# Kernel tuning notes

Measured on AMD Instinct MI355X. Metric: run time of the kernel, lower is better.

## Reference

```python
import jax, jax.numpy as jnp
import numpy as np

EMBED_DIM = 1024
NUM_HEADS = 16
DEPTH = EMBED_DIM // NUM_HEADS  # 64
B, S = 4, 2048


def setup_inputs() -> dict:
    key = jax.random.key(0)
    ks = jax.random.split(key, 12)
    sc = 0.02
    return {
        "q": jax.random.normal(ks[0], (B, S, EMBED_DIM), jnp.float32),
        "k": jax.random.normal(ks[1], (B, S, EMBED_DIM), jnp.float32),
        "v": jax.random.normal(ks[2], (B, S, EMBED_DIM), jnp.float32),
        # per-head Dense(depth) weights stacked over heads: [H, D, depth]
        "wq": jax.random.normal(ks[3], (NUM_HEADS, EMBED_DIM, DEPTH), jnp.float32) * sc,
        "bq": jnp.zeros((NUM_HEADS, DEPTH), jnp.float32),
        "wk": jax.random.normal(ks[4], (NUM_HEADS, EMBED_DIM, DEPTH), jnp.float32) * sc,
        "bk": jnp.zeros((NUM_HEADS, DEPTH), jnp.float32),
        "wv": jax.random.normal(ks[5], (NUM_HEADS, EMBED_DIM, DEPTH), jnp.float32) * sc,
        "bv": jnp.zeros((NUM_HEADS, DEPTH), jnp.float32),
        # final Dense(embedding_dim): [D, D]
        "wo": jax.random.normal(ks[6], (EMBED_DIM, EMBED_DIM), jnp.float32) * sc,
        "bo": jnp.zeros((EMBED_DIM,), jnp.float32),
        "use_mask": 1,
    }


def reference(q, k, v, wq, bq, wk, bk, wv, bv, wo, bo, use_mask):
    # Batched per-head projections (equivalent to H separate Dense layers).
    qh = jnp.einsum('bsd,hde->bhse', q, wq) + bq[None, :, None, :]
    kh = jnp.einsum('bsd,hde->bhse', k, wk) + bk[None, :, None, :]
    vh = jnp.einsum('bsd,hde->bhse', v, wv) + bv[None, :, None, :]

    scale = 1.0 / jnp.sqrt(jnp.asarray(DEPTH, jnp.float32))
    logits = jnp.einsum('bhqe,bhke->bhqk', qh, kh) * scale  # [B,H,Sq,Sk]
    if use_mask:
        Sq, Sk = qh.shape[2], kh.shape[2]
        causal = jnp.triu(jnp.ones((Sq, Sk), jnp.float32), k=1)
        logits = logits + causal[None, None, :, :] * (-1e9)
    attn = jax.nn.softmax(logits, axis=-1)
    out_h = jnp.einsum('bhqk,bhke->bhqe', attn, vh)  # [B,H,Sq,depth]
    # concat heads along last dim -> [B,Sq,H*depth]
    bsz, H, Sq, dep = out_h.shape
    concat = out_h.transpose(0, 2, 1, 3).reshape(bsz, Sq, H * dep)
    return concat @ wo + bo
```

## Files before the change

### kernel.cpp

```cpp
#include <hip/hip_runtime.h>

#define B_ 4
#define S_ 2048
#define H_ 16
#define D_ 64
#define E_ 1024
#define M_ 8192

typedef __attribute__((ext_vector_type(8))) __bf16 bf16x8;
typedef __attribute__((ext_vector_type(4))) __bf16 bf16x4;
typedef __attribute__((ext_vector_type(4))) float f32x4;
typedef __attribute__((ext_vector_type(16))) float f32x16;

__device__ __forceinline__ void gload_lds16(const void* g, void* l) {
  __builtin_amdgcn_global_load_lds(
      (const __attribute__((address_space(1))) unsigned int*)g,
      (__attribute__((address_space(3))) unsigned int*)l, 16, 0, 0);
}

__device__ __forceinline__ unsigned pk2(float a, float b) {
  union { __bf16 h; unsigned short u; } ua, ub;
  ua.h = (__bf16)a; ub.h = (__bf16)b;
  return ((unsigned)ub.u << 16) | (unsigned)ua.u;
}

__global__ void cvt_all(const float* __restrict__ q, const float* __restrict__ k,
                        const float* __restrict__ v, __bf16* __restrict__ Aq,
                        __bf16* __restrict__ Ak, __bf16* __restrict__ Av) {
  const int y = blockIdx.y;
  const float* src = (y == 0) ? q : (y == 1) ? k : v;
  __bf16* dst = (y == 0) ? Aq : (y == 1) ? Ak : Av;
  const int i = blockIdx.x * blockDim.x + threadIdx.x;
  const float4 vv = ((const float4*)src)[i];
  bf16x4 o;
  o.x = (__bf16)vv.x; o.y = (__bf16)vv.y; o.z = (__bf16)vv.z; o.w = (__bf16)vv.w;
  ((bf16x4*)dst)[i] = o;
}

__global__ void pack_all(const float* __restrict__ wq, const float* __restrict__ wk,
                         const float* __restrict__ wv, const float* __restrict__ wo,
                         __bf16* __restrict__ Bq, __bf16* __restrict__ Bk,
                         __bf16* __restrict__ Bv, __bf16* __restrict__ Bo) {
  const int y = blockIdx.y;
  const int idx = blockIdx.x * 256 + threadIdx.x;
  const int n = idx >> 10, kk = idx & 1023;
  if (y < 3) {
    const float* w = (y == 0) ? wq : (y == 1) ? wk : wv;
    __bf16* out = (y == 0) ? Bq : (y == 1) ? Bk : Bv;
    out[idx] = (__bf16)w[((size_t)(n >> 6) << 16) + (kk << 6) + (n & 63)];
  } else {
    Bo[idx] = (__bf16)wo[((size_t)kk << 10) + n];
  }
}

__global__ __launch_bounds__(256) void gemm_qk(
    const __bf16* __restrict__ Aq, const __bf16* __restrict__ Ak,
    const __bf16* __restrict__ Bq, const __bf16* __restrict__ Bk,
    const float* __restrict__ bq, const float* __restrict__ bk,
    __bf16* __restrict__ qhb, __bf16* __restrict__ khb) {
  constexpr int K = 1024;
  __shared__ __bf16 As[128 * 64];
  __shared__ __bf16 Bs[128 * 64];
  const int t = threadIdx.x;
  const int w = t >> 6, l = t & 63;
  const int isK = blockIdx.y >> 3;
  const __bf16* A = isK ? Ak : Aq;
  const __bf16* Bt = isK ? Bk : Bq;
  const float* bias = isK ? bk : bq;
  __bf16* C = isK ? khb : qhb;
  const int m0 = blockIdx.x * 128, n0 = (blockIdx.y & 7) * 128;
  f32x4 acc[4][4] = {};

  for (int kt = 0; kt < K / 64; ++kt) {
    const int kb = kt * 64;
#pragma unroll
    for (int j = 0; j < 4; ++j) {
      const int ci = (j * 4 + w) * 64 + l;
      const int row = ci >> 3;
      const int c = (ci & 7) ^ (row & 7);
      gload_lds16(A + (size_t)(m0 + row) * K + kb + c * 8, As + (j * 4 + w) * 512);
      gload_lds16(Bt + (size_t)(n0 + row) * K + kb + c * 8, Bs + (j * 4 + w) * 512);
    }
    __syncthreads();
#pragma unroll
    for (int kk = 0; kk < 64; kk += 32) {
      bf16x8 af[4], bfr[4];
#pragma unroll
      for (int f = 0; f < 4; ++f) {
        const int ra = (w >> 1) * 64 + f * 16 + (l & 15);
        const int ca = ((kk >> 3) + (l >> 4)) ^ (ra & 7);
        af[f] = *(const bf16x8*)(As + ra * 64 + ca * 8);
        const int rb = (w & 1) * 64 + f * 16 + (l & 15);
        const int cb = ((kk >> 3) + (l >> 4)) ^ (rb & 7);
        bfr[f] = *(const bf16x8*)(Bs + rb * 64 + cb * 8);
      }
#pragma unroll
      for (int mf = 0; mf < 4; ++mf)
#pragma unroll
        for (int nf = 0; nf < 4; ++nf)
          acc[mf][nf] = __builtin_amdgcn_mfma_f32_16x16x32_bf16(af[mf], bfr[nf],
                                                                acc[mf][nf], 0, 0, 0);
    }
    __syncthreads();
  }

#pragma unroll
  for (int mf = 0; mf < 4; ++mf)
#pragma unroll
    for (int nf = 0; nf < 4; ++nf)
#pragma unroll
      for (int r = 0; r < 4; ++r) {
        const int gm = m0 + (w >> 1) * 64 + mf * 16 + (l >> 4) * 4 + r;
        const int gn = n0 + (w & 1) * 64 + nf * 16 + (l & 15);
        const float val = acc[mf][nf][r] + bias[gn];
        C[(((size_t)(gm >> 11) * H_ + (gn >> 6)) * S_ + (gm & 2047)) * D_ + (gn & 63)] =
            (__bf16)val;
      }
}

template <int MODE>
__global__ __launch_bounds__(256) void gemm_bt(const __bf16* __restrict__ A,
                                               const __bf16* __restrict__ Bt,
                                               const float* __restrict__ bias,
                                               void* __restrict__ Cout) {
  constexpr int K = 1024;
  __shared__ __bf16 As[128 * 64];
  __shared__ __bf16 Bs[128 * 64];
  const int t = threadIdx.x;
  const int w = t >> 6, l = t & 63;
  const int m0 = blockIdx.x * 128, n0 = blockIdx.y * 128;
  f32x4 acc[4][4] = {};

  for (int kt = 0; kt < K / 64; ++kt) {
    const int kb = kt * 64;
#pragma unroll
    for (int j = 0; j < 4; ++j) {
      const int ci = (j * 4 + w) * 64 + l;
      const int row = ci >> 3;
      const int c = (ci & 7) ^ (row & 7);
      gload_lds16(A + (size_t)(m0 + row) * K + kb + c * 8, As + (j * 4 + w) * 512);
      gload_lds16(Bt + (size_t)(n0 + row) * K + kb + c * 8, Bs + (j * 4 + w) * 512);
    }
    __syncthreads();
#pragma unroll
    for (int kk = 0; kk < 64; kk += 32) {
      bf16x8 af[4], bfr[4];
#pragma unroll
      for (int f = 0; f < 4; ++f) {
        const int ra = (w >> 1) * 64 + f * 16 + (l & 15);
        const int ca = ((kk >> 3) + (l >> 4)) ^ (ra & 7);
        af[f] = *(const bf16x8*)(As + ra * 64 + ca * 8);
        const int rb = (w & 1) * 64 + f * 16 + (l & 15);
        const int cb = ((kk >> 3) + (l >> 4)) ^ (rb & 7);
        bfr[f] = *(const bf16x8*)(Bs + rb * 64 + cb * 8);
      }
#pragma unroll
      for (int mf = 0; mf < 4; ++mf)
#pragma unroll
        for (int nf = 0; nf < 4; ++nf)
          acc[mf][nf] = __builtin_amdgcn_mfma_f32_16x16x32_bf16(af[mf], bfr[nf],
                                                                acc[mf][nf], 0, 0, 0);
    }
    __syncthreads();
  }

#pragma unroll
  for (int mf = 0; mf < 4; ++mf) {
#pragma unroll
    for (int nf = 0; nf < 4; ++nf) {
#pragma unroll
      for (int r = 0; r < 4; ++r) {
        const int gm = m0 + (w >> 1) * 64 + mf * 16 + (l >> 4) * 4 + r;
        const int gn = n0 + (w & 1) * 64 + nf * 16 + (l & 15);
        const float val = acc[mf][nf][r] + ((MODE == 1) ? bias[gm] : bias[gn]);
        if constexpr (MODE == 1) {
          ((__bf16*)Cout)[(((size_t)(gn >> 11) * H_ + (gm >> 6)) * D_ + (gm & 63)) * S_ + (gn & 2047)] =
              (__bf16)val;
        } else {
          ((float*)Cout)[(size_t)gm * 1024 + gn] = val;
        }
      }
    }
  }
}

__global__ __launch_bounds__(256, 2) void attn_fused(const __bf16* __restrict__ qh,
                                                     const __bf16* __restrict__ kh,
                                                     const __bf16* __restrict__ vT,
                                                     __bf16* __restrict__ concat,
                                                     const int* __restrict__ use_mask_p) {
  __shared__ __bf16 Ks[2][64 * 64];
  __shared__ __bf16 Vs[2][64 * 64];
  const int t = threadIdx.x, w = t >> 6, l = t & 63;
  const int lo = l & 31, hi = l >> 5;
  const int bh = blockIdx.x, pr = blockIdx.y;
  const int usemask = *use_mask_p;
  const __bf16* Qb = qh + (size_t)bh * S_ * D_;
  const __bf16* Kb = kh + (size_t)bh * S_ * D_;
  const __bf16* Vb = vT + (size_t)bh * D_ * S_;
  const int b = bh >> 4, hh = bh & 15;
  constexpr float CEXP = 0.125f * 1.4426950408889634f;

  int cur = 0;
  for (int half = 0; half < 2; ++half) {
    const int qt = half ? (15 - pr) : pr;
    const int qrow0 = qt * 128 + w * 32;
    const int nkt = usemask ? (2 * qt + 2) : (S_ / 64);
    const int ktw = usemask ? (2 * qt + (w >> 1)) : 100000;
    const int ktdiag = usemask ? (2 * qt + (w >> 1)) : -1;

    bf16x8 qf[4];
#pragma unroll
    for (int ks = 0; ks < 4; ++ks)
      qf[ks] = *(const bf16x8*)(Qb + (size_t)(qrow0 + lo) * D_ + ks * 16 + hi * 8);

    float m = -3e38f, ls = 0.f;
    f32x16 o0 = {}, o1 = {};

#pragma unroll
    for (int j = 0; j < 2; ++j) {
      const int ci = j * 256 + t;
      const int row = ci >> 3;
      const int sc = (ci & 7) ^ (row & 7);
      gload_lds16(Kb + (size_t)row * D_ + sc * 8, &Ks[cur][j * 2048 + w * 512]);
      gload_lds16(Vb + (size_t)row * S_ + sc * 8, &Vs[cur][j * 2048 + w * 512]);
    }

    for (int kt = 0; kt < nkt; ++kt) {
      __builtin_amdgcn_sched_barrier(0);
      asm volatile("s_waitcnt vmcnt(0)" ::: "memory");
      __builtin_amdgcn_s_barrier();
      __builtin_amdgcn_sched_barrier(0);

      if (kt + 1 < nkt) {
        const int nxt = cur ^ 1;
#pragma unroll
        for (int j = 0; j < 2; ++j) {
          const int ci = j * 256 + t;
          const int row = ci >> 3;
          const int sc = (ci & 7) ^ (row & 7);
          gload_lds16(Kb + (size_t)((kt + 1) * 64 + row) * D_ + sc * 8,
                      &Ks[nxt][j * 2048 + w * 512]);
          gload_lds16(Vb + (size_t)row * S_ + (kt + 1) * 64 + sc * 8,
                      &Vs[nxt][j * 2048 + w * 512]);
        }
      }

      if (kt <= ktw) {
        f32x16 s0 = {}, s1 = {};
        __builtin_amdgcn_s_setprio(1);
#pragma unroll
        for (int ks = 0; ks < 4; ++ks) {
          const int ch = ((ks << 1) | hi) ^ (lo & 7);
          const bf16x8 k0 = *(const bf16x8*)(&Ks[cur][lo * 64 + ch * 8]);
          const bf16x8 k1 = *(const bf16x8*)(&Ks[cur][(32 + lo) * 64 + ch * 8]);
          s0 = __builtin_amdgcn_mfma_f32_32x32x16_bf16(k0, qf[ks], s0, 0, 0, 0);
          s1 = __builtin_amdgcn_mfma_f32_32x32x16_bf16(k1, qf[ks], s1, 0, 0, 0);
        }
        __builtin_amdgcn_s_setprio(0);

        if (kt == ktdiag) {
          const int qloc = ((w & 1) << 5) + lo;
#pragma unroll
          for (int r = 0; r < 16; ++r) {
            const int kv0 = (r & 3) + 8 * (r >> 2) + 4 * hi;
            if (kv0 > qloc) s0[r] = -1e30f;
            if (kv0 + 32 > qloc) s1[r] = -1e30f;
          }
        }

        float pm = s0[0];
#pragma unroll
        for (int r = 1; r < 16; ++r) pm = fmaxf(pm, s0[r]);
#pragma unroll
        for (int r = 0; r < 16; ++r) pm = fmaxf(pm, s1[r]);
        pm = fmaxf(pm, __shfl_xor(pm, 32));

        if (!__all(pm - m <= 64.0f)) {
          const float mn = fmaxf(m, pm);
          const float al = __builtin_amdgcn_exp2f((m - mn) * CEXP);
          m = mn;
          ls *= al;
          o0 *= al;
          o1 *= al;
        }
        const float mneg = -m * CEXP;

        unsigned W0[4][2], W1[4][2];
        float rs0 = 0.f, rs1 = 0.f;
#pragma unroll
        for (int j = 0; j < 4; ++j) {
          float p0 = __builtin_amdgcn_exp2f(__builtin_fmaf(s0[4 * j + 0], CEXP, mneg));
          float p1 = __builtin_amdgcn_exp2f(__builtin_fmaf(s0[4 * j + 1], CEXP, mneg));
          float p2 = __builtin_amdgcn_exp2f(__builtin_fmaf(s0[4 * j + 2], CEXP, mneg));
          float p3 = __builtin_amdgcn_exp2f(__builtin_fmaf(s0[4 * j + 3], CEXP, mneg));
          rs0 += (p0 + p1) + (p2 + p3);
          W0[j][0] = pk2(p0, p1);
          W0[j][1] = pk2(p2, p3);
          float q0 = __builtin_amdgcn_exp2f(__builtin_fmaf(s1[4 * j + 0], CEXP, mneg));
          float q1 = __builtin_amdgcn_exp2f(__builtin_fmaf(s1[4 * j + 1], CEXP, mneg));
          float q2 = __builtin_amdgcn_exp2f(__builtin_fmaf(s1[4 * j + 2], CEXP, mneg));
          float q3 = __builtin_amdgcn_exp2f(__builtin_fmaf(s1[4 * j + 3], CEXP, mneg));
          rs1 += (q0 + q1) + (q2 + q3);
          W1[j][0] = pk2(q0, q1);
          W1[j][1] = pk2(q2, q3);
        }
        float rs = rs0 + rs1;
        rs += __shfl_xor(rs, 32);
        ls += rs;

        bf16x8 pa[4];
#pragma unroll
        for (int ks = 0; ks < 4; ++ks) {
          const int c = ks & 1;
          unsigned x0, x1, y0, y1;
          if ((ks >> 1) == 0) {
            x0 = W0[2 * c][0]; x1 = W0[2 * c][1];
            y0 = W0[2 * c + 1][0]; y1 = W0[2 * c + 1][1];
          } else {
            x0 = W1[2 * c][0]; x1 = W1[2 * c][1];
            y0 = W1[2 * c + 1][0]; y1 = W1[2 * c + 1][1];
          }
          asm volatile("v_permlane32_swap_b32 %0, %1" : "+v"(x0), "+v"(y0));
          asm volatile("v_permlane32_swap_b32 %0, %1" : "+v"(x1), "+v"(y1));
          union { unsigned u[4]; bf16x8 v; } uu;
          uu.u[0] = x0; uu.u[1] = x1; uu.u[2] = y0; uu.u[3] = y1;
          pa[ks] = uu.v;
        }

        __builtin_amdgcn_s_setprio(1);
#pragma unroll
        for (int ks = 0; ks < 4; ++ks) {
          const int ch = ((ks << 1) | hi) ^ (lo & 7);
          const bf16x8 v0 = *(const bf16x8*)(&Vs[cur][lo * 64 + ch * 8]);
          const bf16x8 v1 = *(const bf16x8*)(&Vs[cur][(32 + lo) * 64 + ch * 8]);
          o0 = __builtin_amdgcn_mfma_f32_32x32x16_bf16(v0, pa[ks], o0, 0, 0, 0);
          o1 = __builtin_amdgcn_mfma_f32_32x32x16_bf16(v1, pa[ks], o1, 0, 0, 0);
        }
        __builtin_amdgcn_s_setprio(0);
      }
      cur ^= 1;
    }

    const float inv = 1.0f / ls;
    const size_t rowbase = ((size_t)(b * S_ + qrow0 + lo)) * E_ + hh * 64;
#pragma unroll
    for (int rr = 0; rr < 4; ++rr) {
      bf16x4 v0, v1;
#pragma unroll
      for (int bb = 0; bb < 4; ++bb) {
        v0[bb] = (__bf16)(o0[4 * rr + bb] * inv);
        v1[bb] = (__bf16)(o1[4 * rr + bb] * inv);
      }
      *(bf16x4*)(concat + rowbase + 8 * rr + 4 * hi) = v0;
      *(bf16x4*)(concat + rowbase + 32 + 8 * rr + 4 * hi) = v1;
    }
  }
}

extern "C" void kernel_launch(void* const* d_in, const int* in_sizes, int n_in,
                              void* d_out, int out_size, void* d_ws, size_t ws_size,
                              hipStream_t stream) {
  const float* q = (const float*)d_in[0];
  const float* k = (const float*)d_in[1];
  const float* v = (const float*)d_in[2];
  const float* wq = (const float*)d_in[3];
  const float* bq = (const float*)d_in[4];
  const float* wk = (const float*)d_in[5];
  const float* bk = (const float*)d_in[6];
  const float* wv = (const float*)d_in[7];
  const float* bv = (const float*)d_in[8];
  const float* wo = (const float*)d_in[9];
  const float* bo = (const float*)d_in[10];
  const int* use_mask = (const int*)d_in[11];
  (void)in_sizes; (void)n_in; (void)out_size; (void)ws_size;

  char* ws = (char*)d_ws;
  __bf16* Aq = (__bf16*)ws;
  __bf16* Ak = Aq + (size_t)M_ * E_;
  __bf16* Av = Ak + (size_t)M_ * E_;
  __bf16* Bq = Av + (size_t)M_ * E_;
  __bf16* Bk = Bq + (size_t)E_ * E_;
  __bf16* Bv = Bk + (size_t)E_ * E_;
  __bf16* Bo = Bv + (size_t)E_ * E_;
  __bf16* qhb = Bo + (size_t)E_ * E_;
  __bf16* khb = qhb + (size_t)8388608;
  __bf16* vTb = khb + (size_t)8388608;
  __bf16* concat = Aq;

  cvt_all<<<dim3(8192, 3), 256, 0, stream>>>(q, k, v, Aq, Ak, Av);
  pack_all<<<dim3(4096, 4), 256, 0, stream>>>(wq, wk, wv, wo, Bq, Bk, Bv, Bo);
  gemm_qk<<<dim3(64, 16), 256, 0, stream>>>(Aq, Ak, Bq, Bk, bq, bk, qhb, khb);
  gemm_bt<1><<<dim3(8, 64), 256, 0, stream>>>(Bv, Av, bv, vTb);
  attn_fused<<<dim3(64, 8), 256, 0, stream>>>(qhb, khb, vTb, concat, use_mask);
  gemm_bt<2><<<dim3(64, 8), 256, 0, stream>>>(concat, Bo, bo, d_out);
}
```

Before: 197.9 us.

## Merge Q/K/V projection GEMMs into one launch and split attention into one q-tile per block

The V-projection GEMM is folded into the Q/K projection kernel as a third grid segment, so the three projections run in one 1536-block launch instead of two. The attention kernel no longer pairs a light and a heavy causal q-tile inside each block. It launches one block per q-tile (1024 blocks), with heavy tiles scheduled first by reversing blockIdx.y. This aims to cut launch overhead and improve load balance and occupancy, but gives up the explicit pairing that kept per-block causal work even.

Result: slower. 208.6 us (+5.4%).

```diff
diff --git a/kernel.cpp b/kernel.cpp
--- a/kernel.cpp
+++ b/kernel.cpp
@@ -53,24 +53,29 @@
   }
 }
 
-__global__ __launch_bounds__(256) void gemm_qk(
+__global__ __launch_bounds__(256) void gemm_qkv(
     const __bf16* __restrict__ Aq, const __bf16* __restrict__ Ak,
-    const __bf16* __restrict__ Bq, const __bf16* __restrict__ Bk,
+    const __bf16* __restrict__ Av, const __bf16* __restrict__ Bq,
+    const __bf16* __restrict__ Bk, const __bf16* __restrict__ Bv,
     const float* __restrict__ bq, const float* __restrict__ bk,
-    __bf16* __restrict__ qhb, __bf16* __restrict__ khb) {
+    const float* __restrict__ bv, __bf16* __restrict__ qhb,
+    __bf16* __restrict__ khb, __bf16* __restrict__ vTb) {
   constexpr int K = 1024;
   __shared__ __bf16 As[128 * 64];
   __shared__ __bf16 Bs[128 * 64];
   const int t = threadIdx.x;
   const int w = t >> 6, l = t & 63;
-  const int isK = blockIdx.y >> 3;
-  const __bf16* A = isK ? Ak : Aq;
-  const __bf16* Bt = isK ? Bk : Bq;
-  const float* bias = isK ? bk : bq;
-  __bf16* C = isK ? khb : qhb;
-  const int m0 = blockIdx.x * 128, n0 = (blockIdx.y & 7) * 128;
+  const int seg = blockIdx.y >> 3;
+  const int yy = blockIdx.y & 7;
+  const __bf16 *A, *Bt;
+  const float* bias;
+  __bf16* C;
+  int m0, n0;
+  if (seg == 0) { A = Aq; Bt = Bq; bias = bq; C = qhb; m0 = blockIdx.x * 128; n0 = yy * 128; }
+  else if (seg == 1) { A = Ak; Bt = Bk; bias = bk; C = khb; m0 = blockIdx.x * 128; n0 = yy * 128; }
+  else { A = Bv; Bt = Av; bias = bv; C = vTb; m0 = yy * 128; n0 = blockIdx.x * 128; }
+
   f32x4 acc[4][4] = {};
-
   for (int kt = 0; kt < K / 64; ++kt) {
     const int kb = kt * 64;
 #pragma unroll
@@ -105,24 +110,31 @@
   }
 
 #pragma unroll
-  for (int mf = 0; mf < 4; ++mf)
-#pragma unroll
-    for (int nf = 0; nf < 4; ++nf)
+  for (int mf = 0; mf < 4; ++mf) {
+#pragma unroll
+    for (int nf = 0; nf < 4; ++nf) {
 #pragma unroll
       for (int r = 0; r < 4; ++r) {
         const int gm = m0 + (w >> 1) * 64 + mf * 16 + (l >> 4) * 4 + r;
         const int gn = n0 + (w & 1) * 64 + nf * 16 + (l & 15);
-        const float val = acc[mf][nf][r] + bias[gn];
-        C[(((size_t)(gm >> 11) * H_ + (gn >> 6)) * S_ + (gm & 2047)) * D_ + (gn & 63)] =
-            (__bf16)val;
-      }
-}
-
-template <int MODE>
-__global__ __launch_bounds__(256) void gemm_bt(const __bf16* __restrict__ A,
-                                               const __bf16* __restrict__ Bt,
-                                               const float* __restrict__ bias,
-                                               void* __restrict__ Cout) {
+        if (seg < 2) {
+          const float val = acc[mf][nf][r] + bias[gn];
+          C[(((size_t)(gm >> 11) * H_ + (gn >> 6)) * S_ + (gm & 2047)) * D_ + (gn & 63)] =
+              (__bf16)val;
+        } else {
+          const float val = acc[mf][nf][r] + bias[gm];
+          C[(((size_t)(gn >> 11) * H_ + (gm >> 6)) * D_ + (gm & 63)) * S_ + (gn & 2047)] =
+              (__bf16)val;
+        }
+      }
+    }
+  }
+}
+
+__global__ __launch_bounds__(256) void out_gemm(const __bf16* __restrict__ A,
+                                                const __bf16* __restrict__ Bt,
+                                                const float* __restrict__ bias,
+                                                float* __restrict__ Cout) {
   constexpr int K = 1024;
   __shared__ __bf16 As[128 * 64];
   __shared__ __bf16 Bs[128 * 64];
@@ -165,23 +177,15 @@
   }
 
 #pragma unroll
-  for (int mf = 0; mf < 4; ++mf) {
-#pragma unroll
-    for (int nf = 0; nf < 4; ++nf) {
+  for (int mf = 0; mf < 4; ++mf)
+#pragma unroll
+    for (int nf = 0; nf < 4; ++nf)
 #pragma unroll
       for (int r = 0; r < 4; ++r) {
         const int gm = m0 + (w >> 1) * 64 + mf * 16 + (l >> 4) * 4 + r;
         const int gn = n0 + (w & 1) * 64 + nf * 16 + (l & 15);
-        const float val = acc[mf][nf][r] + ((MODE == 1) ? bias[gm] : bias[gn]);
-        if constexpr (MODE == 1) {
-          ((__bf16*)Cout)[(((size_t)(gn >> 11) * H_ + (gm >> 6)) * D_ + (gm & 63)) * S_ + (gn & 2047)] =
-              (__bf16)val;
-        } else {
-          ((float*)Cout)[(size_t)gm * 1024 + gn] = val;
-        }
-      }
-    }
-  }
+        Cout[(size_t)gm * 1024 + gn] = acc[mf][nf][r] + bias[gn];
+      }
 }
 
 __global__ __launch_bounds__(256, 2) void attn_fused(const __bf16* __restrict__ qh,
@@ -193,7 +197,8 @@
   __shared__ __bf16 Vs[2][64 * 64];
   const int t = threadIdx.x, w = t >> 6, l = t & 63;
   const int lo = l & 31, hi = l >> 5;
-  const int bh = blockIdx.x, pr = blockIdx.y;
+  const int bh = blockIdx.x;
+  const int qt = 15 - blockIdx.y;
   const int usemask = *use_mask_p;
   const __bf16* Qb = qh + (size_t)bh * S_ * D_;
   const __bf16* Kb = kh + (size_t)bh * S_ * D_;
@@ -201,160 +206,157 @@
   const int b = bh >> 4, hh = bh & 15;
   constexpr float CEXP = 0.125f * 1.4426950408889634f;
 
+  const int qrow0 = qt * 128 + w * 32;
+  const int nkt = usemask ? (2 * qt + 2) : (S_ / 64);
+  const int ktw = usemask ? (2 * qt + (w >> 1)) : 100000;
+  const int ktdiag = usemask ? (2 * qt + (w >> 1)) : -1;
+
+  bf16x8 qf[4];
+#pragma unroll
+  for (int ks = 0; ks < 4; ++ks)
+    qf[ks] = *(const bf16x8*)(Qb + (size_t)(qrow0 + lo) * D_ + ks * 16 + hi * 8);
+
+  float m = -3e38f, ls = 0.f;
+  f32x16 o0 = {}, o1 = {};
   int cur = 0;
-  for (int half = 0; half < 2; ++half) {
-    const int qt = half ? (15 - pr) : pr;
-    const int qrow0 = qt * 128 + w * 32;
-    const int nkt = usemask ? (2 * qt + 2) : (S_ / 64);
-    const int ktw = usemask ? (2 * qt + (w >> 1)) : 100000;
-    const int ktdiag = usemask ? (2 * qt + (w >> 1)) : -1;
-
-    bf16x8 qf[4];
-#pragma unroll
-    for (int ks = 0; ks < 4; ++ks)
-      qf[ks] = *(const bf16x8*)(Qb + (size_t)(qrow0 + lo) * D_ + ks * 16 + hi * 8);
-
-    float m = -3e38f, ls = 0.f;
-    f32x16 o0 = {}, o1 = {};
-
-#pragma unroll
-    for (int j = 0; j < 2; ++j) {
-      const int ci = j * 256 + t;
-      const int row = ci >> 3;
-      const int sc = (ci & 7) ^ (row & 7);
-      gload_lds16(Kb + (size_t)row * D_ + sc * 8, &Ks[cur][j * 2048 + w * 512]);
-      gload_lds16(Vb + (size_t)row * S_ + sc * 8, &Vs[cur][j * 2048 + w * 512]);
-    }
-
-    for (int kt = 0; kt < nkt; ++kt) {
-      __builtin_amdgcn_sched_barrier(0);
-      asm volatile("s_waitcnt vmcnt(0)" ::: "memory");
-      __builtin_amdgcn_s_barrier();
-      __builtin_amdgcn_sched_barrier(0);
-
-      if (kt + 1 < nkt) {
-        const int nxt = cur ^ 1;
-#pragma unroll
-        for (int j = 0; j < 2; ++j) {
-          const int ci = j * 256 + t;
-          const int row = ci >> 3;
-          const int sc = (ci & 7) ^ (row & 7);
-          gload_lds16(Kb + (size_t)((kt + 1) * 64 + row) * D_ + sc * 8,
-                      &Ks[nxt][j * 2048 + w * 512]);
-          gload_lds16(Vb + (size_t)row * S_ + (kt + 1) * 64 + sc * 8,
-                      &Vs[nxt][j * 2048 + w * 512]);
+
+#pragma unroll
+  for (int j = 0; j < 2; ++j) {
+    const int ci = j * 256 + t;
+    const int row = ci >> 3;
+    const int sc = (ci & 7) ^ (row & 7);
+    gload_lds16(Kb + (size_t)row * D_ + sc * 8, &Ks[cur][j * 2048 + w * 512]);
+    gload_lds16(Vb + (size_t)row * S_ + sc * 8, &Vs[cur][j * 2048 + w * 512]);
+  }
+
+  for (int kt = 0; kt < nkt; ++kt) {
+    __builtin_amdgcn_sched_barrier(0);
+    asm volatile("s_waitcnt vmcnt(0)" ::: "memory");
+    __builtin_amdgcn_s_barrier();
+    __builtin_amdgcn_sched_barrier(0);
+
+    if (kt + 1 < nkt) {
+      const int nxt = cur ^ 1;
+#pragma unroll
+      for (int j = 0; j < 2; ++j) {
+        const int ci = j * 256 + t;
+        const int row = ci >> 3;
+        const int sc = (ci & 7) ^ (row & 7);
+        gload_lds16(Kb + (size_t)((kt + 1) * 64 + row) * D_ + sc * 8,
+                    &Ks[nxt][j * 2048 + w * 512]);
+        gload_lds16(Vb + (size_t)row * S_ + (kt + 1) * 64 + sc * 8,
+                    &Vs[nxt][j * 2048 + w * 512]);
+      }
+    }
+
+    if (kt <= ktw) {
+      f32x16 s0 = {}, s1 = {};
+      __builtin_amdgcn_s_setprio(1);
+#pragma unroll
+      for (int ks = 0; ks < 4; ++ks) {
+        const int ch = ((ks << 1) | hi) ^ (lo & 7);
+        const bf16x8 k0 = *(const bf16x8*)(&Ks[cur][lo * 64 + ch * 8]);
+        const bf16x8 k1 = *(const bf16x8*)(&Ks[cur][(32 + lo) * 64 + ch * 8]);
+        s0 = __builtin_amdgcn_mfma_f32_32x32x16_bf16(k0, qf[ks], s0, 0, 0, 0);
+        s1 = __builtin_amdgcn_mfma_f32_32x32x16_bf16(k1, qf[ks], s1, 0, 0, 0);
+      }
+      __builtin_amdgcn_s_setprio(0);
+
+      if (kt == ktdiag) {
+        const int qloc = ((w & 1) << 5) + lo;
+#pragma unroll
+        for (int r = 0; r < 16; ++r) {
+          const int kv0 = (r & 3) + 8 * (r >> 2) + 4 * hi;
+          if (kv0 > qloc) s0[r] = -1e30f;
+          if (kv0 + 32 > qloc) s1[r] = -1e30f;
         }
       }
 
-      if (kt <= ktw) {
-        f32x16 s0 = {}, s1 = {};
-        __builtin_amdgcn_s_setprio(1);
-#pragma unroll
-        for (int ks = 0; ks < 4; ++ks) {
-          const int ch = ((ks << 1) | hi) ^ (lo & 7);
-          const bf16x8 k0 = *(const bf16x8*)(&Ks[cur][lo * 64 + ch * 8]);
-          const bf16x8 k1 = *(const bf16x8*)(&Ks[cur][(32 + lo) * 64 + ch * 8]);
-          s0 = __builtin_amdgcn_mfma_f32_32x32x16_bf16(k0, qf[ks], s0, 0, 0, 0);
-          s1 = __builtin_amdgcn_mfma_f32_32x32x16_bf16(k1, qf[ks], s1, 0, 0, 0);
+      float pm = s0[0];
+#pragma unroll
+      for (int r = 1; r < 16; ++r) pm = fmaxf(pm, s0[r]);
+#pragma unroll
+      for (int r = 0; r < 16; ++r) pm = fmaxf(pm, s1[r]);
+      pm = fmaxf(pm, __shfl_xor(pm, 32));
+
+      if (!__all(pm - m <= 64.0f)) {
+        const float mn = fmaxf(m, pm);
+        const float al = __builtin_amdgcn_exp2f((m - mn) * CEXP);
+        m = mn;
+        ls *= al;
+        o0 *= al;
+        o1 *= al;
+      }
+      const float mneg = -m * CEXP;
+
+      unsigned W0[4][2], W1[4][2];
+      float rs0 = 0.f, rs1 = 0.f;
+#pragma unroll
+      for (int j = 0; j < 4; ++j) {
+        float p0 = __builtin_amdgcn_exp2f(__builtin_fmaf(s0[4 * j + 0], CEXP, mneg));
+        float p1 = __builtin_amdgcn_exp2f(__builtin_fmaf(s0[4 * j + 1], CEXP, mneg));
+        float p2 = __builtin_amdgcn_exp2f(__builtin_fmaf(s0[4 * j + 2], CEXP, mneg));
+        float p3 = __builtin_amdgcn_exp2f(__builtin_fmaf(s0[4 * j + 3], CEXP, mneg));
+        rs0 += (p0 + p1) + (p2 + p3);
+        W0[j][0] = pk2(p0, p1);
+        W0[j][1] = pk2(p2, p3);
+        float q0 = __builtin_amdgcn_exp2f(__builtin_fmaf(s1[4 * j + 0], CEXP, mneg));
+        float q1 = __builtin_amdgcn_exp2f(__builtin_fmaf(s1[4 * j + 1], CEXP, mneg));
+        float q2 = __builtin_amdgcn_exp2f(__builtin_fmaf(s1[4 * j + 2], CEXP, mneg));
+        float q3 = __builtin_amdgcn_exp2f(__builtin_fmaf(s1[4 * j + 3], CEXP, mneg));
+        rs1 += (q0 + q1) + (q2 + q3);
+        W1[j][0] = pk2(q0, q1);
+        W1[j][1] = pk2(q2, q3);
+      }
+      float rs = rs0 + rs1;
+      rs += __shfl_xor(rs, 32);
+      ls += rs;
+
+      bf16x8 pa[4];
+#pragma unroll
+      for (int ks = 0; ks < 4; ++ks) {
+        const int c = ks & 1;
+        unsigned x0, x1, y0, y1;
+        if ((ks >> 1) == 0) {
+          x0 = W0[2 * c][0]; x1 = W0[2 * c][1];
+          y0 = W0[2 * c + 1][0]; y1 = W0[2 * c + 1][1];
+        } else {
+          x0 = W1[2 * c][0]; x1 = W1[2 * c][1];
+          y0 = W1[2 * c + 1][0]; y1 = W1[2 * c + 1][1];
         }
-        __builtin_amdgcn_s_setprio(0);
-
-        if (kt == ktdiag) {
-          const int qloc = ((w & 1) << 5) + lo;
-#pragma unroll
-          for (int r = 0; r < 16; ++r) {
-            const int kv0 = (r & 3) + 8 * (r >> 2) + 4 * hi;
-            if (kv0 > qloc) s0[r] = -1e30f;
-            if (kv0 + 32 > qloc) s1[r] = -1e30f;
-          }
-        }
-
-        float pm = s0[0];
-#pragma unroll
-        for (int r = 1; r < 16; ++r) pm = fmaxf(pm, s0[r]);
-#pragma unroll
-        for (int r = 0; r < 16; ++r) pm = fmaxf(pm, s1[r]);
-        pm = fmaxf(pm, __shfl_xor(pm, 32));
-
-        if (!__all(pm - m <= 64.0f)) {
-          const float mn = fmaxf(m, pm);
-          const float al = __builtin_amdgcn_exp2f((m - mn) * CEXP);
-          m = mn;
-          ls *= al;
-          o0 *= al;
-          o1 *= al;
-        }
-        const float mneg = -m * CEXP;
-
-        unsigned W0[4][2], W1[4][2];
-        float rs0 = 0.f, rs1 = 0.f;
-#pragma unroll
-        for (int j = 0; j < 4; ++j) {
-          float p0 = __builtin_amdgcn_exp2f(__builtin_fmaf(s0[4 * j + 0], CEXP, mneg));
-          float p1 = __builtin_amdgcn_exp2f(__builtin_fmaf(s0[4 * j + 1], CEXP, mneg));
-          float p2 = __builtin_amdgcn_exp2f(__builtin_fmaf(s0[4 * j + 2], CEXP, mneg));
-          float p3 = __builtin_amdgcn_exp2f(__builtin_fmaf(s0[4 * j + 3], CEXP, mneg));
-          rs0 += (p0 + p1) + (p2 + p3);
-          W0[j][0] = pk2(p0, p1);
-          W0[j][1] = pk2(p2, p3);
-          float q0 = __builtin_amdgcn_exp2f(__builtin_fmaf(s1[4 * j + 0], CEXP, mneg));
-          float q1 = __builtin_amdgcn_exp2f(__builtin_fmaf(s1[4 * j + 1], CEXP, mneg));
-          float q2 = __builtin_amdgcn_exp2f(__builtin_fmaf(s1[4 * j + 2], CEXP, mneg));
-          float q3 = __builtin_amdgcn_exp2f(__builtin_fmaf(s1[4 * j + 3], CEXP, mneg));
-          rs1 += (q0 + q1) + (q2 + q3);
-          W1[j][0] = pk2(q0, q1);
-          W1[j][1] = pk2(q2, q3);
-        }
-        float rs = rs0 + rs1;
-        rs += __shfl_xor(rs, 32);
-        ls += rs;
-
-        bf16x8 pa[4];
-#pragma unroll
-        for (int ks = 0; ks < 4; ++ks) {
-          const int c = ks & 1;
-          unsigned x0, x1, y0, y1;
-          if ((ks >> 1) == 0) {
-            x0 = W0[2 * c][0]; x1 = W0[2 * c][1];
-            y0 = W0[2 * c + 1][0]; y1 = W0[2 * c + 1][1];
-          } else {
-            x0 = W1[2 * c][0]; x1 = W1[2 * c][1];
-            y0 = W1[2 * c + 1][0]; y1 = W1[2 * c + 1][1];
-          }
-          asm volatile("v_permlane32_swap_b32 %0, %1" : "+v"(x0), "+v"(y0));
-          asm volatile("v_permlane32_swap_b32 %0, %1" : "+v"(x1), "+v"(y1));
-          union { unsigned u[4]; bf16x8 v; } uu;
-          uu.u[0] = x0; uu.u[1] = x1; uu.u[2] = y0; uu.u[3] = y1;
-          pa[ks] = uu.v;
-        }
-
-        __builtin_amdgcn_s_setprio(1);
-#pragma unroll
-        for (int ks = 0; ks < 4; ++ks) {
-          const int ch = ((ks << 1) | hi) ^ (lo & 7);
-          const bf16x8 v0 = *(const bf16x8*)(&Vs[cur][lo * 64 + ch * 8]);
-          const bf16x8 v1 = *(const bf16x8*)(&Vs[cur][(32 + lo) * 64 + ch * 8]);
-          o0 = __builtin_amdgcn_mfma_f32_32x32x16_bf16(v0, pa[ks], o0, 0, 0, 0);
-          o1 = __builtin_amdgcn_mfma_f32_32x32x16_bf16(v1, pa[ks], o1, 0, 0, 0);
-        }
-        __builtin_amdgcn_s_setprio(0);
-      }
-      cur ^= 1;
-    }
-
-    const float inv = 1.0f / ls;
-    const size_t rowbase = ((size_t)(b * S_ + qrow0 + lo)) * E_ + hh * 64;
-#pragma unroll
-    for (int rr = 0; rr < 4; ++rr) {
-      bf16x4 v0, v1;
-#pragma unroll
-      for (int bb = 0; bb < 4; ++bb) {
-        v0[bb] = (__bf16)(o0[4 * rr + bb] * inv);
-        v1[bb] = (__bf16)(o1[4 * rr + bb] * inv);
-      }
-      *(bf16x4*)(concat + rowbase + 8 * rr + 4 * hi) = v0;
-      *(bf16x4*)(concat + rowbase + 32 + 8 * rr + 4 * hi) = v1;
-    }
+        asm volatile("v_permlane32_swap_b32 %0, %1" : "+v"(x0), "+v"(y0));
+        asm volatile("v_permlane32_swap_b32 %0, %1" : "+v"(x1), "+v"(y1));
+        union { unsigned u[4]; bf16x8 v; } uu;
+        uu.u[0] = x0; uu.u[1] = x1; uu.u[2] = y0; uu.u[3] = y1;
+        pa[ks] = uu.v;
+      }
+
+      __builtin_amdgcn_s_setprio(1);
+#pragma unroll
+      for (int ks = 0; ks < 4; ++ks) {
+        const int ch = ((ks << 1) | hi) ^ (lo & 7);
+        const bf16x8 v0 = *(const bf16x8*)(&Vs[cur][lo * 64 + ch * 8]);
+        const bf16x8 v1 = *(const bf16x8*)(&Vs[cur][(32 + lo) * 64 + ch * 8]);
+        o0 = __builtin_amdgcn_mfma_f32_32x32x16_bf16(v0, pa[ks], o0, 0, 0, 0);
+        o1 = __builtin_amdgcn_mfma_f32_32x32x16_bf16(v1, pa[ks], o1, 0, 0, 0);
+      }
+      __builtin_amdgcn_s_setprio(0);
+    }
+    cur ^= 1;
+  }
+
+  const float inv = 1.0f / ls;
+  const size_t rowbase = ((size_t)(b * S_ + qrow0 + lo)) * E_ + hh * 64;
+#pragma unroll
+  for (int rr = 0; rr < 4; ++rr) {
+    bf16x4 v0, v1;
+#pragma unroll
+    for (int bb = 0; bb < 4; ++bb) {
+      v0[bb] = (__bf16)(o0[4 * rr + bb] * inv);
+      v1[bb] = (__bf16)(o1[4 * rr + bb] * inv);
+    }
+    *(bf16x4*)(concat + rowbase + 8 * rr + 4 * hi) = v0;
+    *(bf16x4*)(concat + rowbase + 32 + 8 * rr + 4 * hi) = v1;
   }
 }
 
@@ -390,8 +392,8 @@
 
   cvt_all<<<dim3(8192, 3), 256, 0, stream>>>(q, k, v, Aq, Ak, Av);
   pack_all<<<dim3(4096, 4), 256, 0, stream>>>(wq, wk, wv, wo, Bq, Bk, Bv, Bo);
-  gemm_qk<<<dim3(64, 16), 256, 0, stream>>>(Aq, Ak, Bq, Bk, bq, bk, qhb, khb);
-  gemm_bt<1><<<dim3(8, 64), 256, 0, stream>>>(Bv, Av, bv, vTb);
-  attn_fused<<<dim3(64, 8), 256, 0, stream>>>(qhb, khb, vTb, concat, use_mask);
-  gemm_bt<2><<<dim3(64, 8), 256, 0, stream>>>(concat, Bo, bo, d_out);
-}
+  gemm_qkv<<<dim3(64, 24), 256, 0, stream>>>(Aq, Ak, Av, Bq, Bk, Bv, bq, bk, bv,
+                                             qhb, khb, vTb);
+  attn_fused<<<dim3(64, 16), 256, 0, stream>>>(qhb, khb, vTb, concat, use_mask);
+  out_gemm<<<dim3(64, 8), 256, 0, stream>>>(concat, Bo, bo, (float*)d_out);
+}
```

## Triple-buffer K/V tiles in attention with two-tile-ahead prefetch

Applied to the files above, without the earlier changes.

Changes the attention kernel's K/V LDS staging from double to triple buffering. Two tiles are issued up front, and each iteration waits only until the current tile has landed (vmcnt(4)) instead of draining every load. The kernel then prefetches tile kt+2, which hides more global-load latency behind the MFMA work. In exchange it uses 48KB of LDS per block, and launch_bounds is raised to 3 blocks, which may limit registers and cause spills.

Result: no change. 196.7 us (-0.6%).

```diff
diff --git a/kernel.cpp b/kernel.cpp
--- a/kernel.cpp
+++ b/kernel.cpp
@@ -184,13 +184,27 @@
   }
 }
 
-__global__ __launch_bounds__(256, 2) void attn_fused(const __bf16* __restrict__ qh,
+__device__ __forceinline__ void stage_tile(const __bf16* __restrict__ Kb,
+                                           const __bf16* __restrict__ Vb,
+                                           int kt, __bf16* Kdst, __bf16* Vdst,
+                                           int t, int w) {
+#pragma unroll
+  for (int j = 0; j < 2; ++j) {
+    const int ci = j * 256 + t;
+    const int row = ci >> 3;
+    const int sc = (ci & 7) ^ (row & 7);
+    gload_lds16(Kb + (size_t)(kt * 64 + row) * D_ + sc * 8, Kdst + j * 2048 + w * 512);
+    gload_lds16(Vb + (size_t)row * S_ + kt * 64 + sc * 8, Vdst + j * 2048 + w * 512);
+  }
+}
+
+__global__ __launch_bounds__(256, 3) void attn_fused(const __bf16* __restrict__ qh,
                                                      const __bf16* __restrict__ kh,
                                                      const __bf16* __restrict__ vT,
                                                      __bf16* __restrict__ concat,
                                                      const int* __restrict__ use_mask_p) {
-  __shared__ __bf16 Ks[2][64 * 64];
-  __shared__ __bf16 Vs[2][64 * 64];
+  __shared__ __bf16 Ks[3][64 * 64];
+  __shared__ __bf16 Vs[3][64 * 64];
   const int t = threadIdx.x, w = t >> 6, l = t & 63;
   const int lo = l & 31, hi = l >> 5;
   const int bh = blockIdx.x, pr = blockIdx.y;
@@ -217,33 +231,26 @@
     float m = -3e38f, ls = 0.f;
     f32x16 o0 = {}, o1 = {};
 
-#pragma unroll
-    for (int j = 0; j < 2; ++j) {
-      const int ci = j * 256 + t;
-      const int row = ci >> 3;
-      const int sc = (ci & 7) ^ (row & 7);
-      gload_lds16(Kb + (size_t)row * D_ + sc * 8, &Ks[cur][j * 2048 + w * 512]);
-      gload_lds16(Vb + (size_t)row * S_ + sc * 8, &Vs[cur][j * 2048 + w * 512]);
+    {
+      const int b1 = (cur + 1 >= 3) ? cur + 1 - 3 : cur + 1;
+      stage_tile(Kb, Vb, 0, &Ks[cur][0], &Vs[cur][0], t, w);
+      stage_tile(Kb, Vb, 1, &Ks[b1][0], &Vs[b1][0], t, w);
     }
 
     for (int kt = 0; kt < nkt; ++kt) {
       __builtin_amdgcn_sched_barrier(0);
-      asm volatile("s_waitcnt vmcnt(0)" ::: "memory");
+      if (kt + 1 < nkt) {
+        asm volatile("s_waitcnt vmcnt(4)" ::: "memory");
+      } else {
+        asm volatile("s_waitcnt vmcnt(0)" ::: "memory");
+      }
       __builtin_amdgcn_s_barrier();
       __builtin_amdgcn_sched_barrier(0);
 
-      if (kt + 1 < nkt) {
-        const int nxt = cur ^ 1;
-#pragma unroll
-        for (int j = 0; j < 2; ++j) {
-          const int ci = j * 256 + t;
-          const int row = ci >> 3;
-          const int sc = (ci & 7) ^ (row & 7);
-          gload_lds16(Kb + (size_t)((kt + 1) * 64 + row) * D_ + sc * 8,
-                      &Ks[nxt][j * 2048 + w * 512]);
-          gload_lds16(Vb + (size_t)row * S_ + (kt + 1) * 64 + sc * 8,
-                      &Vs[nxt][j * 2048 + w * 512]);
-        }
+      if (kt + 2 < nkt) {
+        int tgt = cur + 2;
+        if (tgt >= 3) tgt -= 3;
+        stage_tile(Kb, Vb, kt + 2, &Ks[tgt][0], &Vs[tgt][0], t, w);
       }
 
       if (kt <= ktw) {
@@ -339,7 +346,7 @@
         }
         __builtin_amdgcn_s_setprio(0);
       }
-      cur ^= 1;
+      cur = (cur == 2) ? 0 : cur + 1;
     }
 
     const float inv = 1.0f / ls;
```

## Stage 128-key tiles per barrier and compute row sums via MFMA with ones

Applied to the files above, without the earlier changes.

Each pipeline stage now loads 128 keys and values into LDS, split into two 64-key subtiles, which halves the number of barrier/waitcnt synchronisations per query tile. The softmax row sum is no longer reduced with VALU adds and a cross-lane shuffle; an extra MFMA against a vector of ones accumulates it in matrix registers. The shuffle for the max is moved inside the rare rescale branch. The cost is double the LDS footprint (64KB per block, which may limit occupancy at 2 blocks/CU), an extra MFMA per k-step, and more accumulator registers. Row sums are also taken from bf16-rounded probabilities rather than fp32 values.

Measured after the change: 196.0 us. About the same (-1.0%).

```diff
diff --git a/kernel.cpp b/kernel.cpp
--- a/kernel.cpp
+++ b/kernel.cpp
@@ -184,13 +184,34 @@
   }
 }
 
+__device__ __forceinline__ void stage_k128(const __bf16* __restrict__ Kb, int kt,
+                                           __bf16* Kdst, int t, int w) {
+#pragma unroll
+  for (int j = 0; j < 4; ++j) {
+    const int ci = j * 256 + t;
+    const int row = ci >> 3;
+    const int sc = (ci & 7) ^ (row & 7);
+    gload_lds16(Kb + (size_t)(kt * 128 + row) * D_ + sc * 8, Kdst + j * 2048 + w * 512);
+  }
+}
+__device__ __forceinline__ void stage_v64(const __bf16* __restrict__ Vb, int col0,
+                                          __bf16* Vdst, int t, int w) {
+#pragma unroll
+  for (int j = 0; j < 2; ++j) {
+    const int ci = j * 256 + t;
+    const int row = ci >> 3;
+    const int sc = (ci & 7) ^ (row & 7);
+    gload_lds16(Vb + (size_t)row * S_ + col0 + sc * 8, Vdst + j * 2048 + w * 512);
+  }
+}
+
 __global__ __launch_bounds__(256, 2) void attn_fused(const __bf16* __restrict__ qh,
                                                      const __bf16* __restrict__ kh,
                                                      const __bf16* __restrict__ vT,
                                                      __bf16* __restrict__ concat,
                                                      const int* __restrict__ use_mask_p) {
-  __shared__ __bf16 Ks[2][64 * 64];
-  __shared__ __bf16 Vs[2][64 * 64];
+  __shared__ __bf16 Ks[2][128 * 64];
+  __shared__ __bf16 Vs[2][2][64 * 64];
   const int t = threadIdx.x, w = t >> 6, l = t & 63;
   const int lo = l & 31, hi = l >> 5;
   const int bh = blockIdx.x, pr = blockIdx.y;
@@ -201,30 +222,29 @@
   const int b = bh >> 4, hh = bh & 15;
   constexpr float CEXP = 0.125f * 1.4426950408889634f;
 
+  bf16x8 ones;
+#pragma unroll
+  for (int i = 0; i < 8; ++i) ones[i] = (__bf16)1.0f;
+
   int cur = 0;
   for (int half = 0; half < 2; ++half) {
     const int qt = half ? (15 - pr) : pr;
     const int qrow0 = qt * 128 + w * 32;
-    const int nkt = usemask ? (2 * qt + 2) : (S_ / 64);
-    const int ktw = usemask ? (2 * qt + (w >> 1)) : 100000;
-    const int ktdiag = usemask ? (2 * qt + (w >> 1)) : -1;
+    const int nkt = usemask ? (qt + 1) : (S_ / 128);
+    const int ktw = usemask ? (2 * qt + (w >> 1)) : (1 << 30);
 
     bf16x8 qf[4];
 #pragma unroll
     for (int ks = 0; ks < 4; ++ks)
       qf[ks] = *(const bf16x8*)(Qb + (size_t)(qrow0 + lo) * D_ + ks * 16 + hi * 8);
 
-    float m = -3e38f, ls = 0.f;
+    float m = -3e38f;
+    f32x16 lsacc = {};
     f32x16 o0 = {}, o1 = {};
 
-#pragma unroll
-    for (int j = 0; j < 2; ++j) {
-      const int ci = j * 256 + t;
-      const int row = ci >> 3;
-      const int sc = (ci & 7) ^ (row & 7);
-      gload_lds16(Kb + (size_t)row * D_ + sc * 8, &Ks[cur][j * 2048 + w * 512]);
-      gload_lds16(Vb + (size_t)row * S_ + sc * 8, &Vs[cur][j * 2048 + w * 512]);
-    }
+    stage_k128(Kb, 0, &Ks[cur][0], t, w);
+    stage_v64(Vb, 0, &Vs[cur][0][0], t, w);
+    stage_v64(Vb, 64, &Vs[cur][1][0], t, w);
 
     for (int kt = 0; kt < nkt; ++kt) {
       __builtin_amdgcn_sched_barrier(0);
@@ -234,115 +254,110 @@
 
       if (kt + 1 < nkt) {
         const int nxt = cur ^ 1;
-#pragma unroll
-        for (int j = 0; j < 2; ++j) {
-          const int ci = j * 256 + t;
-          const int row = ci >> 3;
-          const int sc = (ci & 7) ^ (row & 7);
-          gload_lds16(Kb + (size_t)((kt + 1) * 64 + row) * D_ + sc * 8,
-                      &Ks[nxt][j * 2048 + w * 512]);
-          gload_lds16(Vb + (size_t)row * S_ + (kt + 1) * 64 + sc * 8,
-                      &Vs[nxt][j * 2048 + w * 512]);
+        stage_k128(Kb, kt + 1, &Ks[nxt][0], t, w);
+        stage_v64(Vb, (kt + 1) * 128, &Vs[nxt][0][0], t, w);
+        stage_v64(Vb, (kt + 1) * 128 + 64, &Vs[nxt][1][0], t, w);
+      }
+
+#pragma unroll
+      for (int sub = 0; sub < 2; ++sub) {
+        const int st = 2 * kt + sub;
+        if (st <= ktw) {
+          const __bf16* Ksub = &Ks[cur][sub * 64 * 64];
+          const __bf16* Vsub = &Vs[cur][sub][0];
+
+          f32x16 s0 = {}, s1 = {};
+          __builtin_amdgcn_s_setprio(1);
+#pragma unroll
+          for (int ks = 0; ks < 4; ++ks) {
+            const int ch = ((ks << 1) | hi) ^ (lo & 7);
+            const bf16x8 k0 = *(const bf16x8*)(Ksub + lo * 64 + ch * 8);
+            const bf16x8 k1 = *(const bf16x8*)(Ksub + (32 + lo) * 64 + ch * 8);
+            s0 = __builtin_amdgcn_mfma_f32_32x32x16_bf16(k0, qf[ks], s0, 0, 0, 0);
+            s1 = __builtin_amdgcn_mfma_f32_32x32x16_bf16(k1, qf[ks], s1, 0, 0, 0);
+          }
+          __builtin_amdgcn_s_setprio(0);
+
+          if (usemask && st == ktw) {
+            const int qloc = ((w & 1) << 5) + lo;
+#pragma unroll
+            for (int r = 0; r < 16; ++r) {
+              const int kv0 = (r & 3) + 8 * (r >> 2) + 4 * hi;
+              if (kv0 > qloc) s0[r] = -1e30f;
+              if (kv0 + 32 > qloc) s1[r] = -1e30f;
+            }
+          }
+
+          float pm = s0[0];
+#pragma unroll
+          for (int r = 1; r < 16; ++r) pm = fmaxf(pm, s0[r]);
+#pragma unroll
+          for (int r = 0; r < 16; ++r) pm = fmaxf(pm, s1[r]);
+
+          if (!__all(pm - m <= 64.0f)) {
+            const float pmp = fmaxf(pm, __shfl_xor(pm, 32));
+            const float mn = fmaxf(m, pmp);
+            const float al = __builtin_amdgcn_exp2f((m - mn) * CEXP);
+            m = mn;
+            lsacc[0] *= al;
+            o0 *= al;
+            o1 *= al;
+          }
+          const float mneg = -m * CEXP;
+
+          unsigned W0[4][2], W1[4][2];
+#pragma unroll
+          for (int j = 0; j < 4; ++j) {
+            float p0 = __builtin_amdgcn_exp2f(__builtin_fmaf(s0[4 * j + 0], CEXP, mneg));
+            float p1 = __builtin_amdgcn_exp2f(__builtin_fmaf(s0[4 * j + 1], CEXP, mneg));
+            float p2 = __builtin_amdgcn_exp2f(__builtin_fmaf(s0[4 * j + 2], CEXP, mneg));
+            float p3 = __builtin_amdgcn_exp2f(__builtin_fmaf(s0[4 * j + 3], CEXP, mneg));
+            W0[j][0] = pk2(p0, p1);
+            W0[j][1] = pk2(p2, p3);
+            float q0 = __builtin_amdgcn_exp2f(__builtin_fmaf(s1[4 * j + 0], CEXP, mneg));
+            float q1 = __builtin_amdgcn_exp2f(__builtin_fmaf(s1[4 * j + 1], CEXP, mneg));
+            float q2 = __builtin_amdgcn_exp2f(__builtin_fmaf(s1[4 * j + 2], CEXP, mneg));
+            float q3 = __builtin_amdgcn_exp2f(__builtin_fmaf(s1[4 * j + 3], CEXP, mneg));
+            W1[j][0] = pk2(q0, q1);
+            W1[j][1] = pk2(q2, q3);
+          }
+
+          bf16x8 pa[4];
+#pragma unroll
+          for (int ks = 0; ks < 4; ++ks) {
+            const int c = ks & 1;
+            unsigned x0, x1, y0, y1;
+            if ((ks >> 1) == 0) {
+              x0 = W0[2 * c][0]; x1 = W0[2 * c][1];
+              y0 = W0[2 * c + 1][0]; y1 = W0[2 * c + 1][1];
+            } else {
+              x0 = W1[2 * c][0]; x1 = W1[2 * c][1];
+              y0 = W1[2 * c + 1][0]; y1 = W1[2 * c + 1][1];
+            }
+            asm volatile("v_permlane32_swap_b32 %0, %1" : "+v"(x0), "+v"(y0));
+            asm volatile("v_permlane32_swap_b32 %0, %1" : "+v"(x1), "+v"(y1));
+            union { unsigned u[4]; bf16x8 v; } uu;
+            uu.u[0] = x0; uu.u[1] = x1; uu.u[2] = y0; uu.u[3] = y1;
+            pa[ks] = uu.v;
+          }
+
+          __builtin_amdgcn_s_setprio(1);
+#pragma unroll
+          for (int ks = 0; ks < 4; ++ks) {
+            const int ch = ((ks << 1) | hi) ^ (lo & 7);
+            const bf16x8 v0 = *(const bf16x8*)(Vsub + lo * 64 + ch * 8);
+            const bf16x8 v1 = *(const bf16x8*)(Vsub + (32 + lo) * 64 + ch * 8);
+            o0 = __builtin_amdgcn_mfma_f32_32x32x16_bf16(v0, pa[ks], o0, 0, 0, 0);
+            o1 = __builtin_amdgcn_mfma_f32_32x32x16_bf16(v1, pa[ks], o1, 0, 0, 0);
+            lsacc = __builtin_amdgcn_mfma_f32_32x32x16_bf16(ones, pa[ks], lsacc, 0, 0, 0);
+          }
+          __builtin_amdgcn_s_setprio(0);
         }
       }
-
-      if (kt <= ktw) {
-        f32x16 s0 = {}, s1 = {};
-        __builtin_amdgcn_s_setprio(1);
-#pragma unroll
-        for (int ks = 0; ks < 4; ++ks) {
-          const int ch = ((ks << 1) | hi) ^ (lo & 7);
-          const bf16x8 k0 = *(const bf16x8*)(&Ks[cur][lo * 64 + ch * 8]);
-          const bf16x8 k1 = *(const bf16x8*)(&Ks[cur][(32 + lo) * 64 + ch * 8]);
-          s0 = __builtin_amdgcn_mfma_f32_32x32x16_bf16(k0, qf[ks], s0, 0, 0, 0);
-          s1 = __builtin_amdgcn_mfma_f32_32x32x16_bf16(k1, qf[ks], s1, 0, 0, 0);
-        }
-        __builtin_amdgcn_s_setprio(0);
-
-        if (kt == ktdiag) {
-          const int qloc = ((w & 1) << 5) + lo;
-#pragma unroll
-          for (int r = 0; r < 16; ++r) {
-            const int kv0 = (r & 3) + 8 * (r >> 2) + 4 * hi;
-            if (kv0 > qloc) s0[r] = -1e30f;
-            if (kv0 + 32 > qloc) s1[r] = -1e30f;
-          }
-        }
-
-        float pm = s0[0];
-#pragma unroll
-        for (int r = 1; r < 16; ++r) pm = fmaxf(pm, s0[r]);
-#pragma unroll
-        for (int r = 0; r < 16; ++r) pm = fmaxf(pm, s1[r]);
-        pm = fmaxf(pm, __shfl_xor(pm, 32));
-
-        if (!__all(pm - m <= 64.0f)) {
-          const float mn = fmaxf(m, pm);
-          const float al = __builtin_amdgcn_exp2f((m - mn) * CEXP);
-          m = mn;
-          ls *= al;
-          o0 *= al;
-          o1 *= al;
-        }
-        const float mneg = -m * CEXP;
-
-        unsigned W0[4][2], W1[4][2];
-        float rs0 = 0.f, rs1 = 0.f;
-#pragma unroll
-        for (int j = 0; j < 4; ++j) {
-          float p0 = __builtin_amdgcn_exp2f(__builtin_fmaf(s0[4 * j + 0], CEXP, mneg));
-          float p1 = __builtin_amdgcn_exp2f(__builtin_fmaf(s0[4 * j + 1], CEXP, mneg));
-          float p2 = __builtin_amdgcn_exp2f(__builtin_fmaf(s0[4 * j + 2], CEXP, mneg));
-          float p3 = __builtin_amdgcn_exp2f(__builtin_fmaf(s0[4 * j + 3], CEXP, mneg));
-          rs0 += (p0 + p1) + (p2 + p3);
-          W0[j][0] = pk2(p0, p1);
-          W0[j][1] = pk2(p2, p3);
-          float q0 = __builtin_amdgcn_exp2f(__builtin_fmaf(s1[4 * j + 0], CEXP, mneg));
-          float q1 = __builtin_amdgcn_exp2f(__builtin_fmaf(s1[4 * j + 1], CEXP, mneg));
-          float q2 = __builtin_amdgcn_exp2f(__builtin_fmaf(s1[4 * j + 2], CEXP, mneg));
-          float q3 = __builtin_amdgcn_exp2f(__builtin_fmaf(s1[4 * j + 3], CEXP, mneg));
-          rs1 += (q0 + q1) + (q2 + q3);
-          W1[j][0] = pk2(q0, q1);
-          W1[j][1] = pk2(q2, q3);
-        }
-        float rs = rs0 + rs1;
-        rs += __shfl_xor(rs, 32);
-        ls += rs;
-
-        bf16x8 pa[4];
-#pragma unroll
-        for (int ks = 0; ks < 4; ++ks) {
-          const int c = ks & 1;
-          unsigned x0, x1, y0, y1;
-          if ((ks >> 1) == 0) {
-            x0 = W0[2 * c][0]; x1 = W0[2 * c][1];
-            y0 = W0[2 * c + 1][0]; y1 = W0[2 * c + 1][1];
-          } else {
-            x0 = W1[2 * c][0]; x1 = W1[2 * c][1];
-            y0 = W1[2 * c + 1][0]; y1 = W1[2 * c + 1][1];
-          }
-          asm volatile("v_permlane32_swap_b32 %0, %1" : "+v"(x0), "+v"(y0));
-          asm volatile("v_permlane32_swap_b32 %0, %1" : "+v"(x1), "+v"(y1));
-          union { unsigned u[4]; bf16x8 v; } uu;
-          uu.u[0] = x0; uu.u[1] = x1; uu.u[2] = y0; uu.u[3] = y1;
-          pa[ks] = uu.v;
-        }
-
-        __builtin_amdgcn_s_setprio(1);
-#pragma unroll
-        for (int ks = 0; ks < 4; ++ks) {
-          const int ch = ((ks << 1) | hi) ^ (lo & 7);
-          const bf16x8 v0 = *(const bf16x8*)(&Vs[cur][lo * 64 + ch * 8]);
-          const bf16x8 v1 = *(const bf16x8*)(&Vs[cur][(32 + lo) * 64 + ch * 8]);
-          o0 = __builtin_amdgcn_mfma_f32_32x32x16_bf16(v0, pa[ks], o0, 0, 0, 0);
-          o1 = __builtin_amdgcn_mfma_f32_32x32x16_bf16(v1, pa[ks], o1, 0, 0, 0);
-        }
-        __builtin_amdgcn_s_setprio(0);
-      }
       cur ^= 1;
     }
 
-    const float inv = 1.0f / ls;
+    const float inv = 1.0f / lsacc[0];
     const size_t rowbase = ((size_t)(b * S_ + qrow0 + lo)) * E_ + hh * 64;
 #pragma unroll
     for (int rr = 0; rr < 4; ++rr) {
```
